# Kernel tuning notes

Measured on AMD Instinct MI355X. Metric: run time of the kernel, lower is better.

The kernel has to match this reference:

```python
import jax, jax.numpy as jnp
import numpy as np

# Approximate EMD matching (Fan et al. approxmatch): 10 annealed soft-assignment
# rounds with levels -4^j for j = 7..-1 and level 0 for the final round.
_LEVELS = jnp.asarray([-(4.0 ** j) for j in range(7, -2, -1)] + [0.0], dtype=jnp.float32)


def _approx_match(d2, n, m):
    # d2: [b, n, m] squared pairwise distances
    b = d2.shape[0]
    factorl = max(n, m) / float(n)
    factorr = max(n, m) / float(m)
    remainl0 = jnp.full((b, n), factorl, dtype=d2.dtype)
    remainr0 = jnp.full((b, m), factorr, dtype=d2.dtype)
    match0 = jnp.zeros_like(d2)

    def step(carry, level):
        match, remainl, remainr = carry
        w = jnp.exp(level * d2) * remainr[:, None, :]            # [b,n,m]
        w = w / (jnp.sum(w, axis=-1, keepdims=True) + 1e-9)      # row-normalize
        w = w * remainl[:, :, None]                              # scale by left capacity
        ss2 = jnp.sum(w, axis=1)                                 # [b,m] column mass
        s = jnp.minimum(remainr / (ss2 + 1e-9), 1.0)             # column saturation
        w = w * s[:, None, :]
        match = match + w
        remainl = jnp.maximum(remainl - jnp.sum(w, axis=-1), 0.0)
        remainr = jnp.maximum(remainr - jnp.sum(w, axis=1), 0.0)
        return (match, remainl, remainr), None

    (match, _, _), _ = jax.lax.scan(step, (match0, remainl0, remainr0), _LEVELS)
    return match


def setup_inputs() -> dict:
    key = jax.random.key(0)
    k1, k2 = jax.random.split(key)
    xyz1 = jax.random.normal(k1, (16, 2048, 3), dtype=jnp.float32)
    xyz2 = jax.random.normal(k2, (16, 2048, 3), dtype=jnp.float32)
    return {"xyz1": xyz1, "xyz2": xyz2}


def reference(xyz1, xyz2):
    n, m = xyz1.shape[1], xyz2.shape[1]
    diff = xyz1[:, :, None, :] - xyz2[:, None, :, :]             # [b,n,m,3]
    d2 = jnp.sum(diff * diff, axis=-1)                           # [b,n,m]
    match = _approx_match(d2, n, m)
    dist = jnp.sqrt(jnp.maximum(d2, 1e-12))
    cost = jnp.sum(match * dist, axis=(1, 2))                    # [b]
    return cost
```

## Files before the change

kernel.cpp:

```cpp
#include <hip/hip_runtime.h>
#include <math.h>

#define B 16
#define N 2048
#define M 2048
#define BN (B * N)
#define LOG2E 1.4426950408889634f

#define CJ 128
#define NCH (M / CJ)
#define TPB 64
#define RPT 4
#define RBLK (TPB * RPT)

#define EXP2F(x) __builtin_amdgcn_exp2f(x)
#define SQRTF(x) __builtin_amdgcn_sqrtf(x)

__global__ __launch_bounds__(1024) void k_sort(const float* __restrict__ xyz1,
                                               const float* __restrict__ xyz2,
                                               float4* __restrict__ p1,
                                               float4* __restrict__ p2,
                                               float2* __restrict__ ib,
                                               float2* __restrict__ jb) {
    __shared__ float key[2048];
    __shared__ int sidx[2048];
    const int wg = blockIdx.x;
    const int b = wg & (B - 1);
    const bool second = wg >= B;
    const float* src = second ? xyz2 : xyz1;
    const int tx = threadIdx.x;

    for (int t = tx; t < 2048; t += 1024) {
        key[t] = src[3 * (size_t)(b * 2048 + t)];
        sidx[t] = t;
    }
    __syncthreads();

    for (int k = 2; k <= 2048; k <<= 1) {
        for (int j = k >> 1; j > 0; j >>= 1) {
            int e = 2 * tx - (tx & (j - 1));
            int f = e + j;
            bool asc = ((e & k) == 0);
            float ke = key[e], kf = key[f];
            if ((ke > kf) == asc) {
                int ie = sidx[e], if_ = sidx[f];
                key[e] = kf;
                key[f] = ke;
                sidx[e] = if_;
                sidx[f] = ie;
            }
            __syncthreads();
        }
    }

    float4* dst = second ? p2 : p1;
    for (int t = tx; t < 2048; t += 1024) {
        int o = sidx[t];
        const float* s = src + 3 * (size_t)(b * 2048 + o);
        float x = s[0], y = s[1], z = s[2];
        dst[b * 2048 + t] = make_float4(x, y, z, fmaf(x, x, fmaf(y, y, z * z)));
    }
    if (tx < NCH) {
        float2 bb = make_float2(key[tx * CJ], key[tx * CJ + CJ - 1]);
        (second ? jb : ib)[b * NCH + tx] = bb;
    }
}

__global__ __launch_bounds__(256) void k_init(float* __restrict__ rl0,
                                              float* __restrict__ rr0,
                                              float* __restrict__ rs0,
                                              float* __restrict__ rs2,
                                              float* __restrict__ t1b,
                                              float* __restrict__ ss20,
                                              float* __restrict__ cost) {
    int idx = blockIdx.x * 256 + threadIdx.x;
    rl0[idx] = 1.0f;
    rr0[idx] = 1.0f;
    rs0[idx] = 0.0f;
    rs2[idx] = 0.0f;
    t1b[idx] = 0.0f;
    ss20[idx] = 0.0f;
    if (idx < B) cost[idx] = 0.0f;
}

__global__ __launch_bounds__(TPB, 2) void k_rowsum0(const float4* __restrict__ p1,
                                                    const float4* __restrict__ p2,
                                                    const float2* __restrict__ jb,
                                                    float* __restrict__ rs,
                                                    float c2, float sqD) {
    __shared__ float4 tile4[CJ];
    const int b = blockIdx.z;
    const int tx = threadIdx.x;
    const int base = blockIdx.y * RBLK;
    const int i0 = base + tx;

    for (int t = tx; t < CJ; t += TPB) {
        int gj = b * M + blockIdx.x * CJ + t;
        float4 f = p2[gj];
        tile4[t] = make_float4(f.x, f.y, f.z, c2 * f.w);
    }
    __syncthreads();

    float2 bnd = jb[b * NCH + blockIdx.x];
    float rlo = p1[b * N + base].x;
    float rhi = p1[b * N + base + RBLK - 1].x;
    if ((bnd.x - rhi > sqD) || (rlo - bnd.y > sqD)) return;

    float4 f0 = p1[b * N + i0];
    float4 f1 = p1[b * N + i0 + TPB];
    float4 f2 = p1[b * N + i0 + 2 * TPB];
    float4 f3 = p1[b * N + i0 + 3 * TPB];
    const float m2c = -2.0f * c2;
    float X0 = m2c * f0.x, Y0 = m2c * f0.y, Z0 = m2c * f0.z, n0 = c2 * f0.w;
    float X1 = m2c * f1.x, Y1 = m2c * f1.y, Z1 = m2c * f1.z, n1 = c2 * f1.w;
    float X2 = m2c * f2.x, Y2 = m2c * f2.y, Z2 = m2c * f2.z, n2 = c2 * f2.w;
    float X3 = m2c * f3.x, Y3 = m2c * f3.y, Z3 = m2c * f3.z, n3 = c2 * f3.w;

    float a0 = 0.0f, a1 = 0.0f, a2 = 0.0f, a3 = 0.0f;
#pragma unroll 8
    for (int t = 0; t < CJ; ++t) {
        float4 q4 = tile4[t];
        a0 += EXP2F(fmaf(q4.x, X0, fmaf(q4.y, Y0, fmaf(q4.z, Z0, n0 + q4.w))));
        a1 += EXP2F(fmaf(q4.x, X1, fmaf(q4.y, Y1, fmaf(q4.z, Z1, n1 + q4.w))));
        a2 += EXP2F(fmaf(q4.x, X2, fmaf(q4.y, Y2, fmaf(q4.z, Z2, n2 + q4.w))));
        a3 += EXP2F(fmaf(q4.x, X3, fmaf(q4.y, Y3, fmaf(q4.z, Z3, n3 + q4.w))));
    }
    atomicAdd(&rs[b * N + i0], a0);
    atomicAdd(&rs[b * N + i0 + TPB], a1);
    atomicAdd(&rs[b * N + i0 + 2 * TPB], a2);
    atomicAdd(&rs[b * N + i0 + 3 * TPB], a3);
}

__global__ __launch_bounds__(TPB, 2) void k_colsum(const float4* __restrict__ p1,
                                                   const float4* __restrict__ p2,
                                                   const float2* __restrict__ ib,
                                                   const float* __restrict__ rl_in,
                                                   float* __restrict__ rl_out,
                                                   const float* __restrict__ rs_prev,
                                                   const float* __restrict__ rs_cur,
                                                   float* __restrict__ rs_zero,
                                                   const float* __restrict__ t1_in,
                                                   float* __restrict__ t1_zero,
                                                   const float* __restrict__ rr,
                                                   float* __restrict__ ss2_acc,
                                                   float cS, float sqD) {
    __shared__ float4 tile4[CJ];
    __shared__ float tileA[CJ];
    const int b = blockIdx.z;
    const int tx = threadIdx.x;
    const int base = blockIdx.y * RBLK;
    const int j0 = base + tx;

    for (int t = tx; t < CJ; t += TPB) {
        int gi = b * N + blockIdx.x * CJ + t;
        float4 f = p1[gi];
        float rlo = rl_in[gi];
        float ap = rlo / (rs_prev[gi] + 1e-9f);
        float rln = fmaxf(rlo - ap * t1_in[gi], 0.0f);
        float a = rln / (rs_cur[gi] + 1e-9f);
        tile4[t] = make_float4(f.x, f.y, f.z, cS * f.w);
        tileA[t] = a;
        if (blockIdx.y == 0) {
            rl_out[gi] = rln;
            t1_zero[gi] = 0.0f;
            rs_zero[gi] = 0.0f;
        }
    }
    __syncthreads();

    float2 bnd = ib[b * NCH + blockIdx.x];
    float clo = p2[b * M + base].x;
    float chi = p2[b * M + base + RBLK - 1].x;
    if ((bnd.x - chi > sqD) || (clo - bnd.y > sqD)) return;

    float4 f0 = p2[b * M + j0];
    float4 f1 = p2[b * M + j0 + TPB];
    float4 f2 = p2[b * M + j0 + 2 * TPB];
    float4 f3 = p2[b * M + j0 + 3 * TPB];
    const float m2c = -2.0f * cS;
    float X0 = m2c * f0.x, Y0 = m2c * f0.y, Z0 = m2c * f0.z, n0 = cS * f0.w;
    float X1 = m2c * f1.x, Y1 = m2c * f1.y, Z1 = m2c * f1.z, n1 = cS * f1.w;
    float X2 = m2c * f2.x, Y2 = m2c * f2.y, Z2 = m2c * f2.z, n2 = cS * f2.w;
    float X3 = m2c * f3.x, Y3 = m2c * f3.y, Z3 = m2c * f3.z, n3 = cS * f3.w;

    float a0 = 0.0f, a1 = 0.0f, a2 = 0.0f, a3 = 0.0f;
#pragma unroll 8
    for (int t = 0; t < CJ; ++t) {
        float4 q4 = tile4[t];
        float av = tileA[t];
        a0 = fmaf(EXP2F(fmaf(q4.x, X0, fmaf(q4.y, Y0, fmaf(q4.z, Z0, n0 + q4.w)))), av, a0);
        a1 = fmaf(EXP2F(fmaf(q4.x, X1, fmaf(q4.y, Y1, fmaf(q4.z, Z1, n1 + q4.w)))), av, a1);
        a2 = fmaf(EXP2F(fmaf(q4.x, X2, fmaf(q4.y, Y2, fmaf(q4.z, Z2, n2 + q4.w)))), av, a2);
        a3 = fmaf(EXP2F(fmaf(q4.x, X3, fmaf(q4.y, Y3, fmaf(q4.z, Z3, n3 + q4.w)))), av, a3);
    }
    atomicAdd(&ss2_acc[b * M + j0], a0 * rr[b * M + j0]);
    atomicAdd(&ss2_acc[b * M + j0 + TPB], a1 * rr[b * M + j0 + TPB]);
    atomicAdd(&ss2_acc[b * M + j0 + 2 * TPB], a2 * rr[b * M + j0 + 2 * TPB]);
    atomicAdd(&ss2_acc[b * M + j0 + 3 * TPB], a3 * rr[b * M + j0 + 3 * TPB]);
}

__global__ __launch_bounds__(256) void k_suma(const float* __restrict__ rl_in,
                                              float* __restrict__ rl_out,
                                              const float* __restrict__ rs_prev,
                                              const float* __restrict__ rs_cur,
                                              const float* __restrict__ t1_in,
                                              float* __restrict__ S) {
    __shared__ float red[4];
    const int b = blockIdx.x;
    const int tx = threadIdx.x;
    float s = 0.0f;
#pragma unroll
    for (int k = 0; k < N / 256; ++k) {
        int gi = b * N + k * 256 + tx;
        float rlo = rl_in[gi];
        float ap = rlo / (rs_prev[gi] + 1e-9f);
        float rln = fmaxf(rlo - ap * t1_in[gi], 0.0f);
        rl_out[gi] = rln;
        s += rln / (rs_cur[gi] + 1e-9f);
    }
#pragma unroll
    for (int off = 32; off > 0; off >>= 1)
        s += __shfl_down(s, off, 64);
    if ((tx & 63) == 0) red[tx >> 6] = s;
    __syncthreads();
    if (tx == 0) S[b] = red[0] + red[1] + red[2] + red[3];
}

__global__ __launch_bounds__(256) void k_mulss2(const float* __restrict__ rr,
                                                const float* __restrict__ S,
                                                float* __restrict__ ss2_out) {
    int idx = blockIdx.x * 256 + threadIdx.x;
    ss2_out[idx] = rr[idx] * S[idx >> 11];
}

template <int MODE>
__global__ __launch_bounds__(TPB, 2) void k_fused(const float4* __restrict__ p1,
                                                  const float4* __restrict__ p2,
                                                  const float2* __restrict__ jb,
                                                  const float* __restrict__ rr_in,
                                                  float* __restrict__ rr_out,
                                                  const float* __restrict__ ss2_in,
                                                  float* __restrict__ ss2_zero,
                                                  const float* __restrict__ rl_new,
                                                  const float* __restrict__ rs_cur,
                                                  float* __restrict__ rs_next,
                                                  float* __restrict__ t1_acc,
                                                  float* __restrict__ cost,
                                                  float cS, float rsq, float sqD) {
    __shared__ float4 tile4[CJ];
    __shared__ float2 tile2[CJ];
    const int b = blockIdx.z;
    const int tx = threadIdx.x;
    const int base = blockIdx.y * RBLK;
    const int i0 = base + tx;

    for (int t = tx; t < CJ; t += TPB) {
        int gj = b * M + blockIdx.x * CJ + t;
        float4 f = p2[gj];
        float rrv = rr_in[gj];
        float sv = ss2_in[gj];
        float s = fminf(rrv / (sv + 1e-9f), 1.0f);
        float q = rrv * s;
        float rrn = fmaxf(rrv - sv * s, 0.0f);
        tile4[t] = make_float4(f.x, f.y, f.z, q);
        tile2[t] = make_float2(rrn, cS * f.w);
        if (MODE != 2 && blockIdx.y == 0) {
            rr_out[gj] = rrn;
            ss2_zero[gj] = 0.0f;
        }
    }
    __syncthreads();

    if (MODE == 0) {
        float2 bnd = jb[b * NCH + blockIdx.x];
        float rlo = p1[b * N + base].x;
        float rhi = p1[b * N + base + RBLK - 1].x;
        if ((bnd.x - rhi > sqD) || (rlo - bnd.y > sqD)) return;
    }

    float4 f0 = p1[b * N + i0];
    float4 f1 = p1[b * N + i0 + TPB];
    float4 f2 = p1[b * N + i0 + 2 * TPB];
    float4 f3 = p1[b * N + i0 + 3 * TPB];
    const float m2c = -2.0f * cS;
    float X0 = m2c * f0.x, Y0 = m2c * f0.y, Z0 = m2c * f0.z, n0 = cS * f0.w;
    float X1 = m2c * f1.x, Y1 = m2c * f1.y, Z1 = m2c * f1.z, n1 = cS * f1.w;
    float X2 = m2c * f2.x, Y2 = m2c * f2.y, Z2 = m2c * f2.z, n2 = cS * f2.w;
    float X3 = m2c * f3.x, Y3 = m2c * f3.y, Z3 = m2c * f3.z, n3 = cS * f3.w;

    float T10 = 0.0f, T11 = 0.0f, T12 = 0.0f, T13 = 0.0f;
    float T20 = 0.0f, T21 = 0.0f, T22 = 0.0f, T23 = 0.0f;
    float rs0 = 0.0f, rs1 = 0.0f, rs2v = 0.0f, rs3 = 0.0f;
#pragma unroll 8
    for (int t = 0; t < CJ; ++t) {
        float4 q4 = tile4[t];
        float2 rn = tile2[t];
        float g0 = fmaf(q4.x, X0, fmaf(q4.y, Y0, fmaf(q4.z, Z0, n0 + rn.y)));
        float g1 = fmaf(q4.x, X1, fmaf(q4.y, Y1, fmaf(q4.z, Z1, n1 + rn.y)));
        float g2 = fmaf(q4.x, X2, fmaf(q4.y, Y2, fmaf(q4.z, Z2, n2 + rn.y)));
        float g3 = fmaf(q4.x, X3, fmaf(q4.y, Y3, fmaf(q4.z, Z3, n3 + rn.y)));
        float sd0 = SQRTF(fabsf(g0)), sd1 = SQRTF(fabsf(g1));
        float sd2 = SQRTF(fabsf(g2)), sd3 = SQRTF(fabsf(g3));
        float w0, w1, w2, w3;
        if (MODE == 0) {
            float e0 = EXP2F(g0), e1 = EXP2F(g1), e2 = EXP2F(g2), e3 = EXP2F(g3);
            float s0 = e0 * e0, s1 = e1 * e1, s2 = e2 * e2, s3 = e3 * e3;
            w0 = (s0 * s0) * q4.w;
            w1 = (s1 * s1) * q4.w;
            w2 = (s2 * s2) * q4.w;
            w3 = (s3 * s3) * q4.w;
            rs0 = fmaf(e0, rn.x, rs0);
            rs1 = fmaf(e1, rn.x, rs1);
            rs2v = fmaf(e2, rn.x, rs2v);
            rs3 = fmaf(e3, rn.x, rs3);
        } else if (MODE == 1) {
            w0 = EXP2F(g0) * q4.w;
            w1 = EXP2F(g1) * q4.w;
            w2 = EXP2F(g2) * q4.w;
            w3 = EXP2F(g3) * q4.w;
            rs0 += rn.x;
            rs1 += rn.x;
            rs2v += rn.x;
            rs3 += rn.x;
        } else {
            w0 = q4.w;
            w1 = q4.w;
            w2 = q4.w;
            w3 = q4.w;
        }
        T10 += w0;
        T11 += w1;
        T12 += w2;
        T13 += w3;
        T20 = fmaf(w0, sd0, T20);
        T21 = fmaf(w1, sd1, T21);
        T22 = fmaf(w2, sd2, T22);
        T23 = fmaf(w3, sd3, T23);
    }

    const int gi0 = b * N + i0;
    if (MODE != 2) {
        atomicAdd(&t1_acc[gi0], T10);
        atomicAdd(&t1_acc[gi0 + TPB], T11);
        atomicAdd(&t1_acc[gi0 + 2 * TPB], T12);
        atomicAdd(&t1_acc[gi0 + 3 * TPB], T13);
        atomicAdd(&rs_next[gi0], rs0);
        atomicAdd(&rs_next[gi0 + TPB], rs1);
        atomicAdd(&rs_next[gi0 + 2 * TPB], rs2v);
        atomicAdd(&rs_next[gi0 + 3 * TPB], rs3);
    }

    float aa = rl_new[gi0] / (rs_cur[gi0] + 1e-9f);
    float ab = rl_new[gi0 + TPB] / (rs_cur[gi0 + TPB] + 1e-9f);
    float ac = rl_new[gi0 + 2 * TPB] / (rs_cur[gi0 + 2 * TPB] + 1e-9f);
    float ad = rl_new[gi0 + 3 * TPB] / (rs_cur[gi0 + 3 * TPB] + 1e-9f);
    float contrib = rsq * fmaf(aa, T20, fmaf(ab, T21, fmaf(ac, T22, ad * T23)));
#pragma unroll
    for (int off = 32; off > 0; off >>= 1)
        contrib += __shfl_down(contrib, off, 64);
    if (tx == 0) atomicAdd(&cost[b], contrib);
}

extern "C" void kernel_launch(void* const* d_in, const int* in_sizes, int n_in,
                              void* d_out, int out_size, void* d_ws, size_t ws_size,
                              hipStream_t stream) {
    const float* xyz1 = (const float*)d_in[0];
    const float* xyz2 = (const float*)d_in[1];
    float* cost = (float*)d_out;

    float* ws = (float*)d_ws;
    float* rl[2] = {ws + 0 * BN, ws + 1 * BN};
    float* rr[2] = {ws + 2 * BN, ws + 3 * BN};
    float* rs[3] = {ws + 4 * BN, ws + 5 * BN, ws + 6 * BN};
    float* ss2b[2] = {ws + 7 * BN, ws + 8 * BN};
    float* t1[2] = {ws + 9 * BN, ws + 10 * BN};
    float4* p1 = (float4*)(ws + 11 * BN);
    float4* p2 = (float4*)(ws + 15 * BN);
    float* S = ws + 19 * BN;
    float2* ib = (float2*)(ws + 19 * BN + 64);
    float2* jb = (float2*)(ws + 19 * BN + 64 + 512);

    static const float levels[10] = {-16384.0f, -4096.0f, -1024.0f, -256.0f,
                                     -64.0f,    -16.0f,   -4.0f,    -1.0f,
                                     -0.25f,    0.0f};
    float c2[10], sqD[10];
    for (int l = 0; l < 10; ++l) {
        c2[l] = levels[l] * LOG2E;
        sqD[l] = (l < 9) ? sqrtf(150.0f / fabsf(c2[l])) : 1e30f;
    }

    dim3 grid(NCH, N / RBLK, B);
    dim3 blk(TPB);
    dim3 gs(BN / 256);
    dim3 b256(256);

    k_sort<<<dim3(2 * B), dim3(1024), 0, stream>>>(xyz1, xyz2, p1, p2, ib, jb);
    k_init<<<gs, b256, 0, stream>>>(rl[0], rr[0], rs[0], rs[2], t1[1], ss2b[0], cost);
    k_rowsum0<<<grid, blk, 0, stream>>>(p1, p2, jb, rs[0], c2[0], sqD[0]);

    for (int l = 0; l < 10; ++l) {
        int p = l & 1;
        if (l < 9) {
            k_colsum<<<grid, blk, 0, stream>>>(
                p1, p2, ib, rl[p], rl[1 - p], rs[(l + 2) % 3], rs[l % 3],
                rs[(l + 1) % 3], t1[1 - p], t1[p], rr[p], ss2b[p], c2[l], sqD[l]);
        } else {
            k_suma<<<dim3(B), b256, 0, stream>>>(
                rl[p], rl[1 - p], rs[(l + 2) % 3], rs[l % 3], t1[1 - p], S);
            k_mulss2<<<gs, b256, 0, stream>>>(rr[p], S, ss2b[p]);
        }

        if (l <= 7) {
            float cS = c2[l + 1];
            float rsq = 1.0f / sqrtf(fabsf(cS));
            k_fused<0><<<grid, blk, 0, stream>>>(
                p1, p2, jb, rr[p], rr[1 - p], ss2b[p], ss2b[1 - p], rl[1 - p],
                rs[l % 3], rs[(l + 1) % 3], t1[p], cost, cS, rsq, sqD[l + 1]);
        } else if (l == 8) {
            float cS = c2[8];
            float rsq = 1.0f / sqrtf(fabsf(cS));
            k_fused<1><<<grid, blk, 0, stream>>>(
                p1, p2, jb, rr[p], rr[1 - p], ss2b[p], ss2b[1 - p], rl[1 - p],
                rs[l % 3], rs[(l + 1) % 3], t1[p], cost, cS, rsq, 1e30f);
        } else {
            k_fused<2><<<grid, blk, 0, stream>>>(
                p1, p2, jb, rr[p], rr[1 - p], ss2b[p], ss2b[1 - p], rl[1 - p],
                rs[l % 3], rs[(l + 1) % 3], t1[p], cost, 1.0f, 1.0f, 1e30f);
        }
    }
}
```

Baseline: 616.1 us.

## Fold init and ss2 scaling into neighbours; restructure inner loops into 4x4 batches

Merges the init kernel into extra workgroups of the sort kernel. It also drops the k_mulss2 launch by computing rr*S inline in the final fused kernel. The inner loops of rowsum0, colsum and fused are rewritten to load four tile entries at a time and compute 4x4 blocks of exponents and square roots in separate phases. The goal is fewer launches and more independent transcendental work for the scheduler to interleave, at the cost of more registers per thread.

```diff
diff --git a/kernel.cpp b/kernel.cpp
--- a/kernel.cpp
+++ b/kernel.cpp
@@ -21,14 +21,33 @@
                                                float4* __restrict__ p1,
                                                float4* __restrict__ p2,
                                                float2* __restrict__ ib,
-                                               float2* __restrict__ jb) {
+                                               float2* __restrict__ jb,
+                                               float* __restrict__ rl0,
+                                               float* __restrict__ rr0,
+                                               float* __restrict__ rs0,
+                                               float* __restrict__ rs2,
+                                               float* __restrict__ t1b,
+                                               float* __restrict__ ss20,
+                                               float* __restrict__ cost) {
+    const int wg = blockIdx.x;
+    const int tx = threadIdx.x;
+    if (wg >= 2 * B) {
+        int idx = (wg - 2 * B) * 1024 + tx;
+        rl0[idx] = 1.0f;
+        rr0[idx] = 1.0f;
+        rs0[idx] = 0.0f;
+        rs2[idx] = 0.0f;
+        t1b[idx] = 0.0f;
+        ss20[idx] = 0.0f;
+        if (idx < B) cost[idx] = 0.0f;
+        return;
+    }
+
     __shared__ float key[2048];
     __shared__ int sidx[2048];
-    const int wg = blockIdx.x;
     const int b = wg & (B - 1);
     const bool second = wg >= B;
     const float* src = second ? xyz2 : xyz1;
-    const int tx = threadIdx.x;
 
     for (int t = tx; t < 2048; t += 1024) {
         key[t] = src[3 * (size_t)(b * 2048 + t)];
@@ -66,23 +85,6 @@
     }
 }
 
-__global__ __launch_bounds__(256) void k_init(float* __restrict__ rl0,
-                                              float* __restrict__ rr0,
-                                              float* __restrict__ rs0,
-                                              float* __restrict__ rs2,
-                                              float* __restrict__ t1b,
-                                              float* __restrict__ ss20,
-                                              float* __restrict__ cost) {
-    int idx = blockIdx.x * 256 + threadIdx.x;
-    rl0[idx] = 1.0f;
-    rr0[idx] = 1.0f;
-    rs0[idx] = 0.0f;
-    rs2[idx] = 0.0f;
-    t1b[idx] = 0.0f;
-    ss20[idx] = 0.0f;
-    if (idx < B) cost[idx] = 0.0f;
-}
-
 __global__ __launch_bounds__(TPB, 2) void k_rowsum0(const float4* __restrict__ p1,
                                                     const float4* __restrict__ p2,
                                                     const float2* __restrict__ jb,
@@ -106,29 +108,40 @@
     float rhi = p1[b * N + base + RBLK - 1].x;
     if ((bnd.x - rhi > sqD) || (rlo - bnd.y > sqD)) return;
 
-    float4 f0 = p1[b * N + i0];
-    float4 f1 = p1[b * N + i0 + TPB];
-    float4 f2 = p1[b * N + i0 + 2 * TPB];
-    float4 f3 = p1[b * N + i0 + 3 * TPB];
-    const float m2c = -2.0f * c2;
-    float X0 = m2c * f0.x, Y0 = m2c * f0.y, Z0 = m2c * f0.z, n0 = c2 * f0.w;
-    float X1 = m2c * f1.x, Y1 = m2c * f1.y, Z1 = m2c * f1.z, n1 = c2 * f1.w;
-    float X2 = m2c * f2.x, Y2 = m2c * f2.y, Z2 = m2c * f2.z, n2 = c2 * f2.w;
-    float X3 = m2c * f3.x, Y3 = m2c * f3.y, Z3 = m2c * f3.z, n3 = c2 * f3.w;
-
-    float a0 = 0.0f, a1 = 0.0f, a2 = 0.0f, a3 = 0.0f;
-#pragma unroll 8
-    for (int t = 0; t < CJ; ++t) {
-        float4 q4 = tile4[t];
-        a0 += EXP2F(fmaf(q4.x, X0, fmaf(q4.y, Y0, fmaf(q4.z, Z0, n0 + q4.w))));
-        a1 += EXP2F(fmaf(q4.x, X1, fmaf(q4.y, Y1, fmaf(q4.z, Z1, n1 + q4.w))));
-        a2 += EXP2F(fmaf(q4.x, X2, fmaf(q4.y, Y2, fmaf(q4.z, Z2, n2 + q4.w))));
-        a3 += EXP2F(fmaf(q4.x, X3, fmaf(q4.y, Y3, fmaf(q4.z, Z3, n3 + q4.w))));
-    }
-    atomicAdd(&rs[b * N + i0], a0);
-    atomicAdd(&rs[b * N + i0 + TPB], a1);
-    atomicAdd(&rs[b * N + i0 + 2 * TPB], a2);
-    atomicAdd(&rs[b * N + i0 + 3 * TPB], a3);
+    float X[4], Y[4], Z[4], nn[4];
+#pragma unroll
+    for (int r = 0; r < 4; ++r) {
+        float4 f = p1[b * N + i0 + r * TPB];
+        X[r] = -2.0f * c2 * f.x;
+        Y[r] = -2.0f * c2 * f.y;
+        Z[r] = -2.0f * c2 * f.z;
+        nn[r] = c2 * f.w;
+    }
+
+    float acc[4] = {0.0f, 0.0f, 0.0f, 0.0f};
+    for (int t = 0; t < CJ; t += 4) {
+        float4 cc[4];
+#pragma unroll
+        for (int u = 0; u < 4; ++u) cc[u] = tile4[t + u];
+        float g[4][4];
+#pragma unroll
+        for (int u = 0; u < 4; ++u)
+#pragma unroll
+            for (int r = 0; r < 4; ++r)
+                g[u][r] = fmaf(cc[u].x, X[r],
+                               fmaf(cc[u].y, Y[r], fmaf(cc[u].z, Z[r], nn[r] + cc[u].w)));
+        float e[4][4];
+#pragma unroll
+        for (int u = 0; u < 4; ++u)
+#pragma unroll
+            for (int r = 0; r < 4; ++r) e[u][r] = EXP2F(g[u][r]);
+#pragma unroll
+        for (int u = 0; u < 4; ++u)
+#pragma unroll
+            for (int r = 0; r < 4; ++r) acc[r] += e[u][r];
+    }
+#pragma unroll
+    for (int r = 0; r < 4; ++r) atomicAdd(&rs[b * N + i0 + r * TPB], acc[r]);
 }
 
 __global__ __launch_bounds__(TPB, 2) void k_colsum(const float4* __restrict__ p1,
@@ -173,30 +186,45 @@
     float chi = p2[b * M + base + RBLK - 1].x;
     if ((bnd.x - chi > sqD) || (clo - bnd.y > sqD)) return;
 
-    float4 f0 = p2[b * M + j0];
-    float4 f1 = p2[b * M + j0 + TPB];
-    float4 f2 = p2[b * M + j0 + 2 * TPB];
-    float4 f3 = p2[b * M + j0 + 3 * TPB];
-    const float m2c = -2.0f * cS;
-    float X0 = m2c * f0.x, Y0 = m2c * f0.y, Z0 = m2c * f0.z, n0 = cS * f0.w;
-    float X1 = m2c * f1.x, Y1 = m2c * f1.y, Z1 = m2c * f1.z, n1 = cS * f1.w;
-    float X2 = m2c * f2.x, Y2 = m2c * f2.y, Z2 = m2c * f2.z, n2 = cS * f2.w;
-    float X3 = m2c * f3.x, Y3 = m2c * f3.y, Z3 = m2c * f3.z, n3 = cS * f3.w;
-
-    float a0 = 0.0f, a1 = 0.0f, a2 = 0.0f, a3 = 0.0f;
-#pragma unroll 8
-    for (int t = 0; t < CJ; ++t) {
-        float4 q4 = tile4[t];
-        float av = tileA[t];
-        a0 = fmaf(EXP2F(fmaf(q4.x, X0, fmaf(q4.y, Y0, fmaf(q4.z, Z0, n0 + q4.w)))), av, a0);
-        a1 = fmaf(EXP2F(fmaf(q4.x, X1, fmaf(q4.y, Y1, fmaf(q4.z, Z1, n1 + q4.w)))), av, a1);
-        a2 = fmaf(EXP2F(fmaf(q4.x, X2, fmaf(q4.y, Y2, fmaf(q4.z, Z2, n2 + q4.w)))), av, a2);
-        a3 = fmaf(EXP2F(fmaf(q4.x, X3, fmaf(q4.y, Y3, fmaf(q4.z, Z3, n3 + q4.w)))), av, a3);
-    }
-    atomicAdd(&ss2_acc[b * M + j0], a0 * rr[b * M + j0]);
-    atomicAdd(&ss2_acc[b * M + j0 + TPB], a1 * rr[b * M + j0 + TPB]);
-    atomicAdd(&ss2_acc[b * M + j0 + 2 * TPB], a2 * rr[b * M + j0 + 2 * TPB]);
-    atomicAdd(&ss2_acc[b * M + j0 + 3 * TPB], a3 * rr[b * M + j0 + 3 * TPB]);
+    float X[4], Y[4], Z[4], nn[4];
+#pragma unroll
+    for (int r = 0; r < 4; ++r) {
+        float4 f = p2[b * M + j0 + r * TPB];
+        X[r] = -2.0f * cS * f.x;
+        Y[r] = -2.0f * cS * f.y;
+        Z[r] = -2.0f * cS * f.z;
+        nn[r] = cS * f.w;
+    }
+
+    float acc[4] = {0.0f, 0.0f, 0.0f, 0.0f};
+    for (int t = 0; t < CJ; t += 4) {
+        float4 cc[4];
+        float av[4];
+#pragma unroll
+        for (int u = 0; u < 4; ++u) {
+            cc[u] = tile4[t + u];
+            av[u] = tileA[t + u];
+        }
+        float g[4][4];
+#pragma unroll
+        for (int u = 0; u < 4; ++u)
+#pragma unroll
+            for (int r = 0; r < 4; ++r)
+                g[u][r] = fmaf(cc[u].x, X[r],
+                               fmaf(cc[u].y, Y[r], fmaf(cc[u].z, Z[r], nn[r] + cc[u].w)));
+        float e[4][4];
+#pragma unroll
+        for (int u = 0; u < 4; ++u)
+#pragma unroll
+            for (int r = 0; r < 4; ++r) e[u][r] = EXP2F(g[u][r]);
+#pragma unroll
+        for (int u = 0; u < 4; ++u)
+#pragma unroll
+            for (int r = 0; r < 4; ++r) acc[r] = fmaf(e[u][r], av[u], acc[r]);
+    }
+#pragma unroll
+    for (int r = 0; r < 4; ++r)
+        atomicAdd(&ss2_acc[b * M + j0 + r * TPB], acc[r] * rr[b * M + j0 + r * TPB]);
 }
 
 __global__ __launch_bounds__(256) void k_suma(const float* __restrict__ rl_in,
@@ -226,13 +254,6 @@
     if (tx == 0) S[b] = red[0] + red[1] + red[2] + red[3];
 }
 
-__global__ __launch_bounds__(256) void k_mulss2(const float* __restrict__ rr,
-                                                const float* __restrict__ S,
-                                                float* __restrict__ ss2_out) {
-    int idx = blockIdx.x * 256 + threadIdx.x;
-    ss2_out[idx] = rr[idx] * S[idx >> 11];
-}
-
 template <int MODE>
 __global__ __launch_bounds__(TPB, 2) void k_fused(const float4* __restrict__ p1,
                                                   const float4* __restrict__ p2,
@@ -241,6 +262,7 @@
                                                   float* __restrict__ rr_out,
                                                   const float* __restrict__ ss2_in,
                                                   float* __restrict__ ss2_zero,
+                                                  const float* __restrict__ Sb,
                                                   const float* __restrict__ rl_new,
                                                   const float* __restrict__ rs_cur,
                                                   float* __restrict__ rs_next,
@@ -258,7 +280,7 @@
         int gj = b * M + blockIdx.x * CJ + t;
         float4 f = p2[gj];
         float rrv = rr_in[gj];
-        float sv = ss2_in[gj];
+        float sv = (MODE == 2) ? rrv * Sb[b] : ss2_in[gj];
         float s = fminf(rrv / (sv + 1e-9f), 1.0f);
         float q = rrv * s;
         float rrn = fmaxf(rrv - sv * s, 0.0f);
@@ -278,83 +300,95 @@
         if ((bnd.x - rhi > sqD) || (rlo - bnd.y > sqD)) return;
     }
 
-    float4 f0 = p1[b * N + i0];
-    float4 f1 = p1[b * N + i0 + TPB];
-    float4 f2 = p1[b * N + i0 + 2 * TPB];
-    float4 f3 = p1[b * N + i0 + 3 * TPB];
-    const float m2c = -2.0f * cS;
-    float X0 = m2c * f0.x, Y0 = m2c * f0.y, Z0 = m2c * f0.z, n0 = cS * f0.w;
-    float X1 = m2c * f1.x, Y1 = m2c * f1.y, Z1 = m2c * f1.z, n1 = cS * f1.w;
-    float X2 = m2c * f2.x, Y2 = m2c * f2.y, Z2 = m2c * f2.z, n2 = cS * f2.w;
-    float X3 = m2c * f3.x, Y3 = m2c * f3.y, Z3 = m2c * f3.z, n3 = cS * f3.w;
-
-    float T10 = 0.0f, T11 = 0.0f, T12 = 0.0f, T13 = 0.0f;
-    float T20 = 0.0f, T21 = 0.0f, T22 = 0.0f, T23 = 0.0f;
-    float rs0 = 0.0f, rs1 = 0.0f, rs2v = 0.0f, rs3 = 0.0f;
-#pragma unroll 8
-    for (int t = 0; t < CJ; ++t) {
-        float4 q4 = tile4[t];
-        float2 rn = tile2[t];
-        float g0 = fmaf(q4.x, X0, fmaf(q4.y, Y0, fmaf(q4.z, Z0, n0 + rn.y)));
-        float g1 = fmaf(q4.x, X1, fmaf(q4.y, Y1, fmaf(q4.z, Z1, n1 + rn.y)));
-        float g2 = fmaf(q4.x, X2, fmaf(q4.y, Y2, fmaf(q4.z, Z2, n2 + rn.y)));
-        float g3 = fmaf(q4.x, X3, fmaf(q4.y, Y3, fmaf(q4.z, Z3, n3 + rn.y)));
-        float sd0 = SQRTF(fabsf(g0)), sd1 = SQRTF(fabsf(g1));
-        float sd2 = SQRTF(fabsf(g2)), sd3 = SQRTF(fabsf(g3));
-        float w0, w1, w2, w3;
+    float X[4], Y[4], Z[4], nn[4];
+#pragma unroll
+    for (int r = 0; r < 4; ++r) {
+        float4 f = p1[b * N + i0 + r * TPB];
+        X[r] = -2.0f * cS * f.x;
+        Y[r] = -2.0f * cS * f.y;
+        Z[r] = -2.0f * cS * f.z;
+        nn[r] = cS * f.w;
+    }
+
+    float T1[4] = {0, 0, 0, 0}, T2[4] = {0, 0, 0, 0}, rsv[4] = {0, 0, 0, 0};
+    for (int t = 0; t < CJ; t += 4) {
+        float4 cc[4];
+        float2 rn[4];
+#pragma unroll
+        for (int u = 0; u < 4; ++u) {
+            cc[u] = tile4[t + u];
+            rn[u] = tile2[t + u];
+        }
+        float g[4][4];
+#pragma unroll
+        for (int u = 0; u < 4; ++u)
+#pragma unroll
+            for (int r = 0; r < 4; ++r)
+                g[u][r] = fmaf(cc[u].x, X[r],
+                               fmaf(cc[u].y, Y[r], fmaf(cc[u].z, Z[r], nn[r] + rn[u].y)));
+        float sd[4][4];
+#pragma unroll
+        for (int u = 0; u < 4; ++u)
+#pragma unroll
+            for (int r = 0; r < 4; ++r) sd[u][r] = SQRTF(fabsf(g[u][r]));
         if (MODE == 0) {
-            float e0 = EXP2F(g0), e1 = EXP2F(g1), e2 = EXP2F(g2), e3 = EXP2F(g3);
-            float s0 = e0 * e0, s1 = e1 * e1, s2 = e2 * e2, s3 = e3 * e3;
-            w0 = (s0 * s0) * q4.w;
-            w1 = (s1 * s1) * q4.w;
-            w2 = (s2 * s2) * q4.w;
-            w3 = (s3 * s3) * q4.w;
-            rs0 = fmaf(e0, rn.x, rs0);
-            rs1 = fmaf(e1, rn.x, rs1);
-            rs2v = fmaf(e2, rn.x, rs2v);
-            rs3 = fmaf(e3, rn.x, rs3);
+            float e[4][4];
+#pragma unroll
+            for (int u = 0; u < 4; ++u)
+#pragma unroll
+                for (int r = 0; r < 4; ++r) e[u][r] = EXP2F(g[u][r]);
+#pragma unroll
+            for (int u = 0; u < 4; ++u)
+#pragma unroll
+                for (int r = 0; r < 4; ++r) {
+                    float e2 = e[u][r] * e[u][r];
+                    float w = (e2 * e2) * cc[u].w;
+                    T1[r] += w;
+                    T2[r] = fmaf(w, sd[u][r], T2[r]);
+                    rsv[r] = fmaf(e[u][r], rn[u].x, rsv[r]);
+                }
         } else if (MODE == 1) {
-            w0 = EXP2F(g0) * q4.w;
-            w1 = EXP2F(g1) * q4.w;
-            w2 = EXP2F(g2) * q4.w;
-            w3 = EXP2F(g3) * q4.w;
-            rs0 += rn.x;
-            rs1 += rn.x;
-            rs2v += rn.x;
-            rs3 += rn.x;
+            float e[4][4];
+#pragma unroll
+            for (int u = 0; u < 4; ++u)
+#pragma unroll
+                for (int r = 0; r < 4; ++r) e[u][r] = EXP2F(g[u][r]);
+#pragma unroll
+            for (int u = 0; u < 4; ++u)
+#pragma unroll
+                for (int r = 0; r < 4; ++r) {
+                    float w = e[u][r] * cc[u].w;
+                    T1[r] += w;
+                    T2[r] = fmaf(w, sd[u][r], T2[r]);
+                    rsv[r] += rn[u].x;
+                }
         } else {
-            w0 = q4.w;
-            w1 = q4.w;
-            w2 = q4.w;
-            w3 = q4.w;
-        }
-        T10 += w0;
-        T11 += w1;
-        T12 += w2;
-        T13 += w3;
-        T20 = fmaf(w0, sd0, T20);
-        T21 = fmaf(w1, sd1, T21);
-        T22 = fmaf(w2, sd2, T22);
-        T23 = fmaf(w3, sd3, T23);
+#pragma unroll
+            for (int u = 0; u < 4; ++u)
+#pragma unroll
+                for (int r = 0; r < 4; ++r) {
+                    T1[r] += cc[u].w;
+                    T2[r] = fmaf(cc[u].w, sd[u][r], T2[r]);
+                }
+        }
     }
 
     const int gi0 = b * N + i0;
     if (MODE != 2) {
-        atomicAdd(&t1_acc[gi0], T10);
-        atomicAdd(&t1_acc[gi0 + TPB], T11);
-        atomicAdd(&t1_acc[gi0 + 2 * TPB], T12);
-        atomicAdd(&t1_acc[gi0 + 3 * TPB], T13);
-        atomicAdd(&rs_next[gi0], rs0);
-        atomicAdd(&rs_next[gi0 + TPB], rs1);
-        atomicAdd(&rs_next[gi0 + 2 * TPB], rs2v);
-        atomicAdd(&rs_next[gi0 + 3 * TPB], rs3);
-    }
-
-    float aa = rl_new[gi0] / (rs_cur[gi0] + 1e-9f);
-    float ab = rl_new[gi0 + TPB] / (rs_cur[gi0 + TPB] + 1e-9f);
-    float ac = rl_new[gi0 + 2 * TPB] / (rs_cur[gi0 + 2 * TPB] + 1e-9f);
-    float ad = rl_new[gi0 + 3 * TPB] / (rs_cur[gi0 + 3 * TPB] + 1e-9f);
-    float contrib = rsq * fmaf(aa, T20, fmaf(ab, T21, fmaf(ac, T22, ad * T23)));
+#pragma unroll
+        for (int r = 0; r < 4; ++r) {
+            atomicAdd(&t1_acc[gi0 + r * TPB], T1[r]);
+            atomicAdd(&rs_next[gi0 + r * TPB], rsv[r]);
+        }
+    }
+
+    float contrib = 0.0f;
+#pragma unroll
+    for (int r = 0; r < 4; ++r) {
+        float a = rl_new[gi0 + r * TPB] / (rs_cur[gi0 + r * TPB] + 1e-9f);
+        contrib = fmaf(a, T2[r], contrib);
+    }
+    contrib *= rsq;
 #pragma unroll
     for (int off = 32; off > 0; off >>= 1)
         contrib += __shfl_down(contrib, off, 64);
@@ -391,11 +425,10 @@
 
     dim3 grid(NCH, N / RBLK, B);
     dim3 blk(TPB);
-    dim3 gs(BN / 256);
     dim3 b256(256);
 
-    k_sort<<<dim3(2 * B), dim3(1024), 0, stream>>>(xyz1, xyz2, p1, p2, ib, jb);
-    k_init<<<gs, b256, 0, stream>>>(rl[0], rr[0], rs[0], rs[2], t1[1], ss2b[0], cost);
+    k_sort<<<dim3(2 * B + 32), dim3(1024), 0, stream>>>(
+        xyz1, xyz2, p1, p2, ib, jb, rl[0], rr[0], rs[0], rs[2], t1[1], ss2b[0], cost);
     k_rowsum0<<<grid, blk, 0, stream>>>(p1, p2, jb, rs[0], c2[0], sqD[0]);
 
     for (int l = 0; l < 10; ++l) {
@@ -407,25 +440,26 @@
         } else {
             k_suma<<<dim3(B), b256, 0, stream>>>(
                 rl[p], rl[1 - p], rs[(l + 2) % 3], rs[l % 3], t1[1 - p], S);
-            k_mulss2<<<gs, b256, 0, stream>>>(rr[p], S, ss2b[p]);
         }
 
         if (l <= 7) {
             float cS = c2[l + 1];
             float rsq = 1.0f / sqrtf(fabsf(cS));
             k_fused<0><<<grid, blk, 0, stream>>>(
-                p1, p2, jb, rr[p], rr[1 - p], ss2b[p], ss2b[1 - p], rl[1 - p],
-                rs[l % 3], rs[(l + 1) % 3], t1[p], cost, cS, rsq, sqD[l + 1]);
+                p1, p2, jb, rr[p], rr[1 - p], ss2b[p], ss2b[1 - p], nullptr,
+                rl[1 - p], rs[l % 3], rs[(l + 1) % 3], t1[p], cost, cS, rsq,
+                sqD[l + 1]);
         } else if (l == 8) {
             float cS = c2[8];
             float rsq = 1.0f / sqrtf(fabsf(cS));
             k_fused<1><<<grid, blk, 0, stream>>>(
-                p1, p2, jb, rr[p], rr[1 - p], ss2b[p], ss2b[1 - p], rl[1 - p],
-                rs[l % 3], rs[(l + 1) % 3], t1[p], cost, cS, rsq, 1e30f);
+                p1, p2, jb, rr[p], rr[1 - p], ss2b[p], ss2b[1 - p], nullptr,
+                rl[1 - p], rs[l % 3], rs[(l + 1) % 3], t1[p], cost, cS, rsq, 1e30f);
         } else {
             k_fused<2><<<grid, blk, 0, stream>>>(
-                p1, p2, jb, rr[p], rr[1 - p], ss2b[p], ss2b[1 - p], rl[1 - p],
-                rs[l % 3], rs[(l + 1) % 3], t1[p], cost, 1.0f, 1.0f, 1e30f);
-        }
-    }
-}
+                p1, p2, jb, rr[p], rr[1 - p], ss2b[p], ss2b[1 - p], S,
+                rl[1 - p], rs[l % 3], rs[(l + 1) % 3], t1[p], cost, 1.0f, 1.0f,
+                1e30f);
+        }
+    }
+}
```

Result: no change. 627.9 us (+1.9%).
